# Performance work log

Measured on AMD Instinct MI355X. Metric: run time of the kernel, lower is better.

The kernel has to match this reference:

```python
import jax, jax.numpy as jnp
import numpy as np

NUM_EXPERTS = 7
TRUNK_DIM = 64
HIDDEN = 64   # max(48, trunk_dim)
NUM_DEPTH_CLASSES = 3
BATCH = 262144


def setup_inputs() -> dict:
    key = jax.random.key(0)
    ks = jax.random.split(key, 8)
    trunk_feat = jax.random.normal(ks[0], (BATCH, TRUNK_DIM), dtype=jnp.float32)
    size_idx = jax.random.randint(ks[1], (BATCH,), 0, NUM_EXPERTS, dtype=jnp.int64)
    # Stacked expert MLP params: Linear(64,64) -> ReLU -> Linear(64,64) -> ReLU -> Linear(64,3)
    s1 = 1.0 / np.sqrt(TRUNK_DIM)
    s2 = 1.0 / np.sqrt(HIDDEN)
    W1 = jax.random.uniform(ks[2], (NUM_EXPERTS, TRUNK_DIM, HIDDEN), jnp.float32, -s1, s1)
    b1 = jax.random.uniform(ks[3], (NUM_EXPERTS, HIDDEN), jnp.float32, -s1, s1)
    W2 = jax.random.uniform(ks[4], (NUM_EXPERTS, HIDDEN, HIDDEN), jnp.float32, -s2, s2)
    b2 = jax.random.uniform(ks[5], (NUM_EXPERTS, HIDDEN), jnp.float32, -s2, s2)
    W3 = jax.random.uniform(ks[6], (NUM_EXPERTS, HIDDEN, NUM_DEPTH_CLASSES), jnp.float32, -s2, s2)
    b3 = jax.random.uniform(ks[7], (NUM_EXPERTS, NUM_DEPTH_CLASSES), jnp.float32, -s2, s2)
    return {"trunk_feat": trunk_feat, "size_idx": size_idx,
            "W1": W1, "b1": b1, "W2": W2, "b2": b2, "W3": W3, "b3": b3}


def _expert_mlp(x, W1, b1, W2, b2, W3, b3):
    # 3-layer MLP of one expert (dropout = identity in eval mode)
    h = jax.nn.relu(x @ W1 + b1)
    h = jax.nn.relu(h @ W2 + b2)
    return h @ W3 + b3  # [B, num_depth_classes]


def reference(trunk_feat, size_idx, W1, b1, W2, b2, W3, b3):
    # Hard routing (route_logits): rows with size_idx == e go through expert e;
    # expressed as masked accumulate so it is jit-friendly (no data-dependent shapes).
    B = trunk_feat.shape[0]
    logits = jnp.zeros((B, NUM_DEPTH_CLASSES), dtype=trunk_feat.dtype)
    for e in range(NUM_EXPERTS):  # fixed, small expert count
        le = _expert_mlp(trunk_feat, W1[e], b1[e], W2[e], b2[e], W3[e], b3[e])
        mask = (size_idx == e)[:, None]
        logits = logits + jnp.where(mask, le, jnp.zeros_like(le))
    probs = jax.nn.softmax(logits, axis=1)
    return logits, probs
```

## Files before the change

### kernel.cpp

```cpp
#include <hip/hip_runtime.h>
#include <stdint.h>

#define NE    7
#define DD    64
#define NDC   3
#define BLOCK 256
#define ROWS  256
#define NFRAG 18

typedef __fp16   half8 __attribute__((ext_vector_type(8)));
typedef float    f32x4 __attribute__((ext_vector_type(4)));
typedef uint32_t u32x4 __attribute__((ext_vector_type(4)));
typedef uint32_t u32x2 __attribute__((ext_vector_type(2)));
typedef __fp16   h2_t  __attribute__((ext_vector_type(2)));

__device__ __forceinline__ uint32_t pkrtz(float a, float b) {
  h2_t h = __builtin_amdgcn_cvt_pkrtz(a, b);
  return __builtin_bit_cast(uint32_t, h);
}

__device__ __forceinline__ f32x4 mfma16(u32x4 a, u32x4 b, f32x4 c) {
  return __builtin_amdgcn_mfma_f32_16x16x32_f16(
      __builtin_bit_cast(half8, a), __builtin_bit_cast(half8, b), c, 0, 0, 0);
}

__device__ __forceinline__ u32x4 relu_pack(f32x4 lo, f32x4 hi) {
  u32x4 t = { pkrtz(fmaxf(lo[0],0.f), fmaxf(lo[1],0.f)),
              pkrtz(fmaxf(lo[2],0.f), fmaxf(lo[3],0.f)),
              pkrtz(fmaxf(hi[0],0.f), fmaxf(hi[1],0.f)),
              pkrtz(fmaxf(hi[2],0.f), fmaxf(hi[3],0.f)) };
  return t;
}

__global__ __launch_bounds__(BLOCK) void pack_w(
    const float* __restrict__ W1, const float* __restrict__ W2,
    const float* __restrict__ W3, uint32_t* __restrict__ ws) {
  const int e = blockIdx.x;
  const float* Wl0 = W1 + e*DD*DD;
  const float* Wl1 = W2 + e*DD*DD;
  const float* Wl2 = W3 + e*DD*NDC;
  for (int idx = threadIdx.x; idx < NFRAG*64; idx += BLOCK) {
    const int f = idx >> 6, l = idx & 63;
    int layer, fl;
    if (f < 8)       { layer = 0; fl = f; }
    else if (f < 16) { layer = 1; fl = f - 8; }
    else             { layer = 2; fl = f - 16; }
    const int nt = (layer < 2) ? (fl >> 1) : 0;
    const int ks = fl & 1;
    const int n  = nt*16 + (l & 15);
    const int g  = l >> 4;
    uint32_t dst[4];
    for (int d = 0; d < 4; ++d) {
      float v[2];
      for (int h = 0; h < 2; ++h) {
        const int kk = 16*(d>>1) + 4*g + 2*(d&1) + h;
        const int k  = 32*ks + kk;
        float val;
        if (layer == 0)      val = Wl0[k*DD + n];
        else if (layer == 1) val = Wl1[k*DD + n];
        else                 val = (n < NDC) ? Wl2[k*NDC + n] : 0.0f;
        v[h] = val;
      }
      dst[d] = pkrtz(v[0], v[1]);
    }
    uint32_t* p = ws + ((size_t)(e*NFRAG + f)*64 + l)*4;
    p[0]=dst[0]; p[1]=dst[1]; p[2]=dst[2]; p[3]=dst[3];
  }
}

__global__ __launch_bounds__(BLOCK, 3) void fused(
    const float* __restrict__ X, const int* __restrict__ S,
    const u32x4* __restrict__ wf,
    const float* __restrict__ b1, const float* __restrict__ b2,
    const float* __restrict__ b3,
    float* __restrict__ out, int B)
{
  __shared__ uint32_t pk[ROWS*32];
  __shared__ uint16_t srt[ROWS];
  __shared__ int wcnt[4][NE];
  __shared__ int woff[4][NE];
  __shared__ int cnt[NE];

  const int tid  = threadIdx.x;
  const int wv   = tid >> 6, lane = tid & 63;
  const int r15  = lane & 15, g = lane >> 4;
  const int base = blockIdx.x * ROWS;

  const int e_i = S[base + tid];
  unsigned long long mk[NE];
  #pragma unroll
  for (int e = 0; e < NE; ++e) mk[e] = __ballot(e_i == e);
  int myprefix = 0;
  #pragma unroll
  for (int e = 0; e < NE; ++e)
    if (e_i == e) myprefix = __popcll(mk[e] & ((1ull << lane) - 1ull));
  if (lane < NE) wcnt[wv][lane] = __popcll(mk[lane]);
  __syncthreads();

  if (tid == 0) {
    int acc = 0;
    for (int e = 0; e < NE; ++e) {
      const int s0 = acc;
      for (int w = 0; w < 4; ++w) { woff[w][e] = acc; acc += wcnt[w][e]; }
      cnt[e] = acc - s0;
    }
  }
  {
    const float4* Xb = (const float4*)(X + (size_t)base * DD);
    const int q     = lane & 15;
    const int rsub  = lane >> 4;
    const int ksq   = q >> 3, gq = q & 3, hq = (q >> 2) & 1;
    const int slotq = 4*ksq + gq;
    #pragma unroll
    for (int it = 0; it < 16; ++it) {
      const int r = wv*64 + it*4 + rsub;
      const float4 v = Xb[r*16 + q];
      u32x2 w2 = { pkrtz(v.x, v.y), pkrtz(v.z, v.w) };
      *(u32x2*)&pk[r*32 + ((slotq ^ (r & 7)) << 2) + hq*2] = w2;
    }
  }
  __syncthreads();

  srt[woff[wv][e_i] + myprefix] = (uint16_t)tid;
  __syncthreads();

  int pst[NE + 1];
  {
    int tp = 0;
    #pragma unroll
    for (int e = 0; e < NE; ++e) { pst[e] = tp; tp += (cnt[e] + 31) >> 5; }
    pst[NE] = tp;
  }

  for (int p = wv; p < pst[NE]; p += 4) {
    int e = 0;
    #pragma unroll
    for (int q2 = 1; q2 < NE; ++q2) if (p >= pst[q2]) e = q2;
    const int ch    = p - pst[e];
    const int m     = min(32, cnt[e] - ch*32);
    const int sbase = woff[0][e] + ch*32;

    const u32x4* wse = wf + (size_t)e*NFRAG*64;
    u32x4 af[NFRAG];
    #pragma unroll
    for (int f = 0; f < NFRAG; ++f) af[f] = wse[f*64 + lane];

    #pragma unroll 1
    for (int jt = 0; jt < 2; ++jt) {
      const int idx16 = min(jt*16 + r15, m - 1);
      const int lr    = srt[sbase + idx16];

      const u32x4 xf0 = *(const u32x4*)&pk[lr*32 + (((g    ) ^ (lr & 7)) << 2)];
      const u32x4 xf1 = *(const u32x4*)&pk[lr*32 + (((4 + g) ^ (lr & 7)) << 2)];

      f32x4 c[4];
      #pragma unroll
      for (int nt = 0; nt < 4; ++nt) {
        const float4 bv = *(const float4*)(b1 + e*DD + nt*16 + 4*g);
        f32x4 acc = { bv.x, bv.y, bv.z, bv.w };
        acc = mfma16(af[nt*2 + 0], xf0, acc);
        acc = mfma16(af[nt*2 + 1], xf1, acc);
        c[nt] = acc;
      }
      const u32x4 h0 = relu_pack(c[0], c[1]);
      const u32x4 h1 = relu_pack(c[2], c[3]);

      #pragma unroll
      for (int nt = 0; nt < 4; ++nt) {
        const float4 bv = *(const float4*)(b2 + e*DD + nt*16 + 4*g);
        f32x4 acc = { bv.x, bv.y, bv.z, bv.w };
        acc = mfma16(af[8 + nt*2 + 0], h0, acc);
        acc = mfma16(af[8 + nt*2 + 1], h1, acc);
        c[nt] = acc;
      }
      const u32x4 t0 = relu_pack(c[0], c[1]);
      const u32x4 t1 = relu_pack(c[2], c[3]);

      f32x4 acc = { b3[e*NDC + 0], b3[e*NDC + 1], b3[e*NDC + 2], 0.f };
      acc = mfma16(af[16], t0, acc);
      acc = mfma16(af[17], t1, acc);

      if (g == 0 && (jt*16 + r15) < m) {
        const int row = base + lr;
        const float l0 = acc[0], l1 = acc[1], l2 = acc[2];
        const float mx  = fmaxf(l0, fmaxf(l1, l2));
        const float p0  = __expf(l0 - mx);
        const float p1  = __expf(l1 - mx);
        const float p2  = __expf(l2 - mx);
        const float inv = 1.0f / (p0 + p1 + p2);
        float* o = out + (size_t)row*3;
        o[0] = l0; o[1] = l1; o[2] = l2;
        float* pr = out + (size_t)B*3 + (size_t)row*3;
        pr[0] = p0*inv; pr[1] = p1*inv; pr[2] = p2*inv;
      }
    }
  }
}

extern "C" void kernel_launch(void* const* d_in, const int* in_sizes, int n_in,
                              void* d_out, int out_size, void* d_ws, size_t ws_size,
                              hipStream_t stream)
{
  const float* X  = (const float*)d_in[0];
  const int*   S  = (const int*)d_in[1];
  const float* W1 = (const float*)d_in[2];
  const float* B1 = (const float*)d_in[3];
  const float* W2 = (const float*)d_in[4];
  const float* B2 = (const float*)d_in[5];
  const float* W3 = (const float*)d_in[6];
  const float* B3 = (const float*)d_in[7];
  float* out = (float*)d_out;
  uint32_t* ws = (uint32_t*)d_ws;

  const int B = in_sizes[0] / DD;

  pack_w<<<NE, BLOCK, 0, stream>>>(W1, W2, W3, ws);
  fused<<<B / ROWS, BLOCK, 0, stream>>>(X, S, (const u32x4*)ws,
                                        B1, B2, B3, out, B);
}
```

Measured before the change: 36.86 us.

## Halve rows per block, stage outputs in LDS, interleave two tiles, parallelize weight packing

Several changes land together. The block tile shrinks to 128 rows and the occupancy hint goes from 3 to 4. Logits and probabilities are now staged in shared memory so the global writes are coalesced instead of scattered per row. Weight fragments are loaded one layer at a time to cut register pressure, and both 16-row tiles go through each layer together so the MFMA work interleaves. The weight-packing kernel now runs on 14 blocks and stages each matrix in LDS. The costs are more blocks, and only two of four waves doing routing, which adds idle work per block.

```diff
diff --git a/kernel.cpp b/kernel.cpp
--- a/kernel.cpp
+++ b/kernel.cpp
@@ -5,7 +5,7 @@
 #define DD    64
 #define NDC   3
 #define BLOCK 256
-#define ROWS  256
+#define ROWS  128
 #define NFRAG 18
 
 typedef __fp16   half8 __attribute__((ext_vector_type(8)));
@@ -32,43 +32,64 @@
   return t;
 }
 
-__global__ __launch_bounds__(BLOCK) void pack_w(
+__global__ __launch_bounds__(BLOCK) void pack_w2(
     const float* __restrict__ W1, const float* __restrict__ W2,
     const float* __restrict__ W3, uint32_t* __restrict__ ws) {
-  const int e = blockIdx.x;
-  const float* Wl0 = W1 + e*DD*DD;
-  const float* Wl1 = W2 + e*DD*DD;
-  const float* Wl2 = W3 + e*DD*NDC;
-  for (int idx = threadIdx.x; idx < NFRAG*64; idx += BLOCK) {
-    const int f = idx >> 6, l = idx & 63;
-    int layer, fl;
-    if (f < 8)       { layer = 0; fl = f; }
-    else if (f < 16) { layer = 1; fl = f - 8; }
-    else             { layer = 2; fl = f - 16; }
-    const int nt = (layer < 2) ? (fl >> 1) : 0;
-    const int ks = fl & 1;
-    const int n  = nt*16 + (l & 15);
-    const int g  = l >> 4;
+  __shared__ float wt[DD*DD];
+  const int blk = blockIdx.x;
+  const int e = blk >> 1, half = blk & 1;
+  const float* Wsrc = (half ? W2 : W1) + (size_t)e*DD*DD;
+
+  const float4* s4 = (const float4*)Wsrc;
+  float4* d4 = (float4*)wt;
+  #pragma unroll
+  for (int i = 0; i < DD*DD/4/BLOCK; ++i)
+    d4[i*BLOCK + threadIdx.x] = s4[i*BLOCK + threadIdx.x];
+  __syncthreads();
+
+  for (int idx = threadIdx.x; idx < 8*64; idx += BLOCK) {
+    const int fl = idx >> 6, l = idx & 63;
+    const int nt = fl >> 1, ks = fl & 1;
+    const int n  = nt*16 + (l & 15), g = l >> 4;
     uint32_t dst[4];
+    #pragma unroll
     for (int d = 0; d < 4; ++d) {
       float v[2];
+      #pragma unroll
       for (int h = 0; h < 2; ++h) {
         const int kk = 16*(d>>1) + 4*g + 2*(d&1) + h;
-        const int k  = 32*ks + kk;
-        float val;
-        if (layer == 0)      val = Wl0[k*DD + n];
-        else if (layer == 1) val = Wl1[k*DD + n];
-        else                 val = (n < NDC) ? Wl2[k*NDC + n] : 0.0f;
-        v[h] = val;
+        v[h] = wt[(32*ks + kk)*DD + n];
       }
       dst[d] = pkrtz(v[0], v[1]);
     }
-    uint32_t* p = ws + ((size_t)(e*NFRAG + f)*64 + l)*4;
+    uint32_t* p = ws + ((size_t)(e*NFRAG + half*8 + fl)*64 + l)*4;
     p[0]=dst[0]; p[1]=dst[1]; p[2]=dst[2]; p[3]=dst[3];
   }
-}
-
-__global__ __launch_bounds__(BLOCK, 3) void fused(
+
+  if (half == 0) {
+    const float* Wl2 = W3 + (size_t)e*DD*NDC;
+    for (int idx = threadIdx.x; idx < 2*64; idx += BLOCK) {
+      const int ks = idx >> 6, l = idx & 63;
+      const int n  = l & 15, g = l >> 4;
+      uint32_t dst[4];
+      #pragma unroll
+      for (int d = 0; d < 4; ++d) {
+        float v[2];
+        #pragma unroll
+        for (int h = 0; h < 2; ++h) {
+          const int kk = 16*(d>>1) + 4*g + 2*(d&1) + h;
+          const int k  = 32*ks + kk;
+          v[h] = (n < NDC) ? Wl2[k*NDC + n] : 0.0f;
+        }
+        dst[d] = pkrtz(v[0], v[1]);
+      }
+      uint32_t* p = ws + ((size_t)(e*NFRAG + 16 + ks)*64 + l)*4;
+      p[0]=dst[0]; p[1]=dst[1]; p[2]=dst[2]; p[3]=dst[3];
+    }
+  }
+}
+
+__global__ __launch_bounds__(BLOCK, 4) void fused(
     const float* __restrict__ X, const int* __restrict__ S,
     const u32x4* __restrict__ wf,
     const float* __restrict__ b1, const float* __restrict__ b2,
@@ -76,9 +97,10 @@
     float* __restrict__ out, int B)
 {
   __shared__ uint32_t pk[ROWS*32];
+  __shared__ float    outbuf[ROWS*6];
   __shared__ uint16_t srt[ROWS];
-  __shared__ int wcnt[4][NE];
-  __shared__ int woff[4][NE];
+  __shared__ int wcnt[2][NE];
+  __shared__ int woff[2][NE];
   __shared__ int cnt[NE];
 
   const int tid  = threadIdx.x;
@@ -86,22 +108,24 @@
   const int r15  = lane & 15, g = lane >> 4;
   const int base = blockIdx.x * ROWS;
 
-  const int e_i = S[base + tid];
-  unsigned long long mk[NE];
-  #pragma unroll
-  for (int e = 0; e < NE; ++e) mk[e] = __ballot(e_i == e);
-  int myprefix = 0;
-  #pragma unroll
-  for (int e = 0; e < NE; ++e)
-    if (e_i == e) myprefix = __popcll(mk[e] & ((1ull << lane) - 1ull));
-  if (lane < NE) wcnt[wv][lane] = __popcll(mk[lane]);
+  int e_i = 0, myprefix = 0;
+  if (wv < 2) {
+    e_i = S[base + tid];
+    unsigned long long mk[NE];
+    #pragma unroll
+    for (int e = 0; e < NE; ++e) mk[e] = __ballot(e_i == e);
+    #pragma unroll
+    for (int e = 0; e < NE; ++e)
+      if (e_i == e) myprefix = __popcll(mk[e] & ((1ull << lane) - 1ull));
+    if (lane < NE) wcnt[wv][lane] = __popcll(mk[lane]);
+  }
   __syncthreads();
 
   if (tid == 0) {
     int acc = 0;
     for (int e = 0; e < NE; ++e) {
       const int s0 = acc;
-      for (int w = 0; w < 4; ++w) { woff[w][e] = acc; acc += wcnt[w][e]; }
+      for (int w = 0; w < 2; ++w) { woff[w][e] = acc; acc += wcnt[w][e]; }
       cnt[e] = acc - s0;
     }
   }
@@ -112,8 +136,8 @@
     const int ksq   = q >> 3, gq = q & 3, hq = (q >> 2) & 1;
     const int slotq = 4*ksq + gq;
     #pragma unroll
-    for (int it = 0; it < 16; ++it) {
-      const int r = wv*64 + it*4 + rsub;
+    for (int it = 0; it < 8; ++it) {
+      const int r = wv*32 + it*4 + rsub;
       const float4 v = Xb[r*16 + q];
       u32x2 w2 = { pkrtz(v.x, v.y), pkrtz(v.z, v.w) };
       *(u32x2*)&pk[r*32 + ((slotq ^ (r & 7)) << 2) + hq*2] = w2;
@@ -121,7 +145,7 @@
   }
   __syncthreads();
 
-  srt[woff[wv][e_i] + myprefix] = (uint16_t)tid;
+  if (tid < ROWS) srt[woff[wv][e_i] + myprefix] = (uint16_t)tid;
   __syncthreads();
 
   int pst[NE + 1];
@@ -139,61 +163,89 @@
     const int ch    = p - pst[e];
     const int m     = min(32, cnt[e] - ch*32);
     const int sbase = woff[0][e] + ch*32;
+    const int njt   = (m > 16) ? 2 : 1;
 
     const u32x4* wse = wf + (size_t)e*NFRAG*64;
-    u32x4 af[NFRAG];
-    #pragma unroll
-    for (int f = 0; f < NFRAG; ++f) af[f] = wse[f*64 + lane];
-
-    #pragma unroll 1
-    for (int jt = 0; jt < 2; ++jt) {
+
+    u32x4 afA[8];
+    #pragma unroll
+    for (int f = 0; f < 8; ++f) afA[f] = wse[f*64 + lane];
+
+    int lr[2] = {0, 0};
+    u32x4 xf[2][2];
+    #pragma unroll
+    for (int jt = 0; jt < 2; ++jt) {
+      if (jt >= njt) break;
       const int idx16 = min(jt*16 + r15, m - 1);
-      const int lr    = srt[sbase + idx16];
-
-      const u32x4 xf0 = *(const u32x4*)&pk[lr*32 + (((g    ) ^ (lr & 7)) << 2)];
-      const u32x4 xf1 = *(const u32x4*)&pk[lr*32 + (((4 + g) ^ (lr & 7)) << 2)];
-
+      lr[jt] = srt[sbase + idx16];
+      xf[jt][0] = *(const u32x4*)&pk[lr[jt]*32 + (((    g) ^ (lr[jt] & 7)) << 2)];
+      xf[jt][1] = *(const u32x4*)&pk[lr[jt]*32 + (((4 + g) ^ (lr[jt] & 7)) << 2)];
+    }
+
+    u32x4 h[2][2];
+    #pragma unroll
+    for (int jt = 0; jt < 2; ++jt) {
+      if (jt >= njt) break;
       f32x4 c[4];
       #pragma unroll
       for (int nt = 0; nt < 4; ++nt) {
         const float4 bv = *(const float4*)(b1 + e*DD + nt*16 + 4*g);
         f32x4 acc = { bv.x, bv.y, bv.z, bv.w };
-        acc = mfma16(af[nt*2 + 0], xf0, acc);
-        acc = mfma16(af[nt*2 + 1], xf1, acc);
+        acc = mfma16(afA[nt*2 + 0], xf[jt][0], acc);
+        acc = mfma16(afA[nt*2 + 1], xf[jt][1], acc);
         c[nt] = acc;
       }
-      const u32x4 h0 = relu_pack(c[0], c[1]);
-      const u32x4 h1 = relu_pack(c[2], c[3]);
-
+      h[jt][0] = relu_pack(c[0], c[1]);
+      h[jt][1] = relu_pack(c[2], c[3]);
+    }
+
+    #pragma unroll
+    for (int f = 0; f < 8; ++f) afA[f] = wse[(8 + f)*64 + lane];
+
+    u32x4 t[2][2];
+    #pragma unroll
+    for (int jt = 0; jt < 2; ++jt) {
+      if (jt >= njt) break;
+      f32x4 c[4];
       #pragma unroll
       for (int nt = 0; nt < 4; ++nt) {
         const float4 bv = *(const float4*)(b2 + e*DD + nt*16 + 4*g);
         f32x4 acc = { bv.x, bv.y, bv.z, bv.w };
-        acc = mfma16(af[8 + nt*2 + 0], h0, acc);
-        acc = mfma16(af[8 + nt*2 + 1], h1, acc);
+        acc = mfma16(afA[nt*2 + 0], h[jt][0], acc);
+        acc = mfma16(afA[nt*2 + 1], h[jt][1], acc);
         c[nt] = acc;
       }
-      const u32x4 t0 = relu_pack(c[0], c[1]);
-      const u32x4 t1 = relu_pack(c[2], c[3]);
-
+      t[jt][0] = relu_pack(c[0], c[1]);
+      t[jt][1] = relu_pack(c[2], c[3]);
+    }
+
+    const u32x4 a30 = wse[16*64 + lane];
+    const u32x4 a31 = wse[17*64 + lane];
+    #pragma unroll
+    for (int jt = 0; jt < 2; ++jt) {
+      if (jt >= njt) break;
       f32x4 acc = { b3[e*NDC + 0], b3[e*NDC + 1], b3[e*NDC + 2], 0.f };
-      acc = mfma16(af[16], t0, acc);
-      acc = mfma16(af[17], t1, acc);
-
+      acc = mfma16(a30, t[jt][0], acc);
+      acc = mfma16(a31, t[jt][1], acc);
       if (g == 0 && (jt*16 + r15) < m) {
-        const int row = base + lr;
         const float l0 = acc[0], l1 = acc[1], l2 = acc[2];
         const float mx  = fmaxf(l0, fmaxf(l1, l2));
         const float p0  = __expf(l0 - mx);
         const float p1  = __expf(l1 - mx);
         const float p2  = __expf(l2 - mx);
         const float inv = 1.0f / (p0 + p1 + p2);
-        float* o = out + (size_t)row*3;
-        o[0] = l0; o[1] = l1; o[2] = l2;
-        float* pr = out + (size_t)B*3 + (size_t)row*3;
-        pr[0] = p0*inv; pr[1] = p1*inv; pr[2] = p2*inv;
-      }
-    }
+        float* ob = outbuf + lr[jt]*6;
+        ob[0] = l0;      ob[1] = l1;      ob[2] = l2;
+        ob[3] = p0*inv;  ob[4] = p1*inv;  ob[5] = p2*inv;
+      }
+    }
+  }
+  __syncthreads();
+
+  for (int i = tid; i < ROWS*3; i += BLOCK) {
+    const int r = i/3, c2 = i - r*3;
+    out[(size_t)base*3 + i]                = outbuf[r*6 + c2];
+    out[(size_t)B*3 + (size_t)base*3 + i]  = outbuf[r*6 + 3 + c2];
   }
 }
 
@@ -214,7 +266,7 @@
 
   const int B = in_sizes[0] / DD;
 
-  pack_w<<<NE, BLOCK, 0, stream>>>(W1, W2, W3, ws);
+  pack_w2<<<NE*2, BLOCK, 0, stream>>>(W1, W2, W3, ws);
   fused<<<B / ROWS, BLOCK, 0, stream>>>(X, S, (const u32x4*)ws,
                                         B1, B2, B3, out, B);
 }
```

Result: no change. 36.97 us (+0.3%).
